# Optimization experiments

Measured on AMD Instinct MI355X. Metric: run time of the kernel, lower is better.

Reference implementation:

```python
import jax, jax.numpy as jnp
import numpy as np
from jax import lax

B, S, D = 4, 4096, 2048
R, E, K, H = 256, 8, 2, 512
MAX_BLEND = 0.9


def setup_inputs() -> dict:
    key = jax.random.key(0)
    ks = jax.random.split(key, 11)
    def w(k, shape, fan_in):
        return jax.random.normal(k, shape, dtype=jnp.float32) * (1.0 / np.sqrt(fan_in))
    return {
        "h": jax.random.normal(ks[0], (B, S, D), dtype=jnp.float32),
        "V": w(ks[1], (D, R), D),            # down-projection (z = V^T h)
        "U": w(ks[2], (R, D), R),            # reconstruction (h = U z)
        "Wr": w(ks[3], (R, E), R),           # router
        "br": jnp.zeros((E,), dtype=jnp.float32),
        "W1": w(ks[4], (E, R, H), R),        # per-expert up-proj
        "b1": jnp.zeros((E, H), dtype=jnp.float32),
        "W2": w(ks[5], (E, H, R), H),        # per-expert down-proj
        "b2": jnp.zeros((E, R), dtype=jnp.float32),
        "Wh": w(ks[6], (D, 1), D),           # halting unit
        "bh": jnp.zeros((1,), dtype=jnp.float32),
    }


def _forward(h, V, U, Wr, br, W1, b1, W2, b2, Wh, bh):
    b, s, d = h.shape
    T = b * s
    # 1. project to vein subspace: z = V^T h  -> [B,S,R]
    z = jnp.einsum("bsd,dr->bsr", h, V)
    zf = z.reshape(T, R)
    # 2. top-k routing
    logits = zf @ Wr + br                      # [T,E]
    probs = jax.nn.softmax(logits, axis=-1)
    topw, topi = lax.top_k(probs, K)           # [T,K]
    topw = topw / jnp.sum(topw, axis=-1, keepdims=True)
    combine = jnp.zeros((T, E), dtype=zf.dtype).at[jnp.arange(T)[:, None], topi].add(topw)
    # 3. expert mix (dense-compute reference; combine is K-sparse per token)
    hidden = jax.nn.gelu(jnp.einsum("tr,erh->teh", zf, W1) + b1, approximate=False)
    expert_out = jnp.einsum("teh,ehr->ter", hidden, W2) + b2    # [T,E,R]
    z_new = jnp.einsum("te,ter->tr", combine, expert_out).reshape(b, s, R)
    # 4. residual blend: blend = min(top_k/num_experts, max_blend)
    blend = min(K / E, MAX_BLEND)
    z_final = z_new * blend + z * (1.0 - blend)
    # 5. reconstruct + halting
    h_new = jnp.einsum("bsr,rd->bsd", z_final, U)
    p_halt = jax.nn.sigmoid(jnp.einsum("bsd,do->bso", h_new, Wh) + bh)
    return h_new, p_halt


def reference(h, V, U, Wr, br, W1, b1, W2, b2, Wh, bh):
    return _forward(h, V, U, Wr, br, W1, b1, W2, b2, Wh, bh)
```

## Files before the change

kernel.cpp:

```cpp
#include <hip/hip_runtime.h>
#include <stdint.h>
#include <math.h>

#define TK 16384
#define DD 2048
#define RR 256
#define EE 8
#define HH 512
#define NSEG_MAX 264
#define NPAIR_MAX (NSEG_MAX * 128)

typedef __attribute__((ext_vector_type(4))) float f32x4;
typedef __attribute__((ext_vector_type(8))) short s16x8;
typedef __attribute__((ext_vector_type(8))) unsigned short u16x8;
typedef __attribute__((ext_vector_type(4))) unsigned u32x4;
typedef unsigned short ushort_t;

__device__ inline unsigned short f2bf(float f) {
  union { float f; unsigned u; } v; v.f = f;
  unsigned r = v.u + 0x7fffu + ((v.u >> 16) & 1u);
  return (unsigned short)(r >> 16);
}
__device__ inline float bf2f(ushort_t u) {
  union { unsigned u; float f; } v; v.u = ((unsigned)u) << 16; return v.f;
}

__device__ inline void gll16(const void* g, void* l) {
  __builtin_amdgcn_global_load_lds(
      (const __attribute__((address_space(1))) void*)g,
      (__attribute__((address_space(3))) void*)l, 16, 0, 0);
}

__device__ inline u16x8 pack8(f32x4 a, f32x4 b) {
  u16x8 r;
  r[0] = f2bf(a.x); r[1] = f2bf(a.y); r[2] = f2bf(a.z); r[3] = f2bf(a.w);
  r[4] = f2bf(b.x); r[5] = f2bf(b.y); r[6] = f2bf(b.z); r[7] = f2bf(b.w);
  return r;
}

#define SWZ8(idx) (((idx & 7) ^ ((idx >> 3) & 7)) * 8)

__global__ __launch_bounds__(256) void k_prep(
    const float* __restrict__ V, const float* __restrict__ U,
    const float* __restrict__ W1, const float* __restrict__ W2,
    const float* __restrict__ Wr, const float* __restrict__ Wh,
    ushort_t* __restrict__ Vt, ushort_t* __restrict__ Ut,
    ushort_t* __restrict__ W1t, ushort_t* __restrict__ W2t,
    float* __restrict__ VeffT, float* __restrict__ Uh) {
  __shared__ float sm[2112];
  int b = blockIdx.x, t = threadIdx.x;
  if (b < 3072) {
    const float* src; ushort_t* dst; int nr, nc, c0, r0;
    if (b < 512)       { src = V; dst = Vt; nr = 2048; nc = 256;
                         c0 = (b & 7) * 32; r0 = (b >> 3) * 32; }
    else if (b < 1024) { int bx = b - 512; src = U; dst = Ut; nr = 256; nc = 2048;
                         c0 = (bx & 63) * 32; r0 = (bx >> 6) * 32; }
    else if (b < 2048) { int bx = b - 1024; int s = bx >> 7; bx &= 127;
                         src = W1 + (size_t)s * 131072; dst = W1t + (size_t)s * 131072;
                         nr = 256; nc = 512; c0 = (bx & 15) * 32; r0 = (bx >> 4) * 32; }
    else               { int bx = b - 2048; int s = bx >> 7; bx &= 127;
                         src = W2 + (size_t)s * 131072; dst = W2t + (size_t)s * 131072;
                         nr = 512; nc = 256; c0 = (bx & 7) * 32; r0 = (bx >> 3) * 32; }
    int tx = t & 31, ty = t >> 5;
    #pragma unroll
    for (int i = 0; i < 32; i += 8)
      sm[(ty + i) * 33 + tx] = src[(size_t)(r0 + ty + i) * nc + c0 + tx];
    __syncthreads();
    #pragma unroll
    for (int i = 0; i < 32; i += 8)
      dst[(size_t)(c0 + ty + i) * nr + r0 + tx] = f2bf(sm[tx * 33 + ty + i]);
  } else if (b < 3080) {
    #pragma unroll
    for (int i = 0; i < 8; ++i) sm[i * 256 + t] = Wr[i * 256 + t];
    __syncthreads();
    int d = (b - 3072) * 256 + t;
    float a[8] = {0, 0, 0, 0, 0, 0, 0, 0};
    const float* vrow = V + (size_t)d * RR;
    for (int r = 0; r < RR; r += 4) {
      f32x4 v = *(const f32x4*)(vrow + r);
      #pragma unroll
      for (int e = 0; e < 8; ++e)
        a[e] += v.x * sm[r * 8 + e] + v.y * sm[(r + 1) * 8 + e] +
                v.z * sm[(r + 2) * 8 + e] + v.w * sm[(r + 3) * 8 + e];
    }
    #pragma unroll
    for (int e = 0; e < 8; ++e) VeffT[(size_t)e * DD + d] = a[e];
  } else {
    int wave = t >> 6, lane = t & 63;
    int r = (b - 3080) * 4 + wave;
    const f32x4* u4 = (const f32x4*)(U + (size_t)r * DD);
    const f32x4* w4 = (const f32x4*)Wh;
    float acc = 0.f;
    #pragma unroll
    for (int it = 0; it < 8; ++it) {
      f32x4 a = u4[it * 64 + lane], bb = w4[it * 64 + lane];
      acc += a.x * bb.x + a.y * bb.y + a.z * bb.z + a.w * bb.w;
    }
    #pragma unroll
    for (int o = 32; o; o >>= 1) acc += __shfl_down(acc, o, 64);
    if (lane == 0) Uh[r] = acc;
  }
}

__global__ __launch_bounds__(256, 2) void k_front(
    const float* __restrict__ h, const ushort_t* __restrict__ Vt,
    const float* __restrict__ VeffT, const float* __restrict__ br,
    ushort_t* __restrict__ zb, int* __restrict__ topi, float* __restrict__ topw,
    int* __restrict__ ctrl) {
  __shared__ ushort_t As[2][32 * 72];
  __shared__ ushort_t Bs[2][256 * 64];
  __shared__ float Vs[2][512];
  __shared__ int lcnt[8];
  int t = threadIdx.x;
  int m0 = blockIdx.x * 32;
  int lane = t & 63, wave = t >> 6;
  int ln = lane & 15, hi = lane >> 4;
  const int xo = (ln & 7) << 3;
  int arow = t >> 3, koff = (t & 7) * 8;
  const float* aptr = h + (size_t)(m0 + arow) * DD + koff;
  if (t < 8) lcnt[t] = 0;

  f32x4 acc[2][4];
  #pragma unroll
  for (int i = 0; i < 2; ++i)
    #pragma unroll
    for (int j = 0; j < 4; ++j) acc[i][j] = (f32x4){0.f, 0.f, 0.f, 0.f};
  float racc[8] = {0, 0, 0, 0, 0, 0, 0, 0};

  f32x4 pc0, pc1, pn0, pn1;
  {
    pc0 = ((const f32x4*)aptr)[0];
    pc1 = ((const f32x4*)aptr)[1];
    #pragma unroll
    for (int u = 0; u < 8; ++u) {
      int idx = u * 256 + t;
      gll16(Vt + (size_t)(idx >> 3) * DD + SWZ8(idx), &Bs[0][idx * 8]);
    }
    if (t < 128) gll16(VeffT + (size_t)(t >> 4) * DD + (t & 15) * 4, &Vs[0][t * 4]);
    *(u16x8*)&As[0][arow * 72 + koff] = pack8(pc0, pc1);
  }
  __syncthreads();

  for (int s = 0; s < 32; ++s) {
    int cb = s & 1, xb = cb ^ 1;
    int k1 = (s + 1) * 64;
    if (s < 31) {
      pn0 = ((const f32x4*)(aptr + k1))[0];
      pn1 = ((const f32x4*)(aptr + k1))[1];
      #pragma unroll
      for (int u = 0; u < 8; ++u) {
        int idx = u * 256 + t;
        gll16(Vt + (size_t)(idx >> 3) * DD + k1 + SWZ8(idx), &Bs[xb][idx * 8]);
      }
      if (t < 128) gll16(VeffT + (size_t)(t >> 4) * DD + k1 + (t & 15) * 4, &Vs[xb][t * 4]);
    }
    {
      const f32x4* vsb = (const f32x4*)&Vs[cb][0];
      #pragma unroll
      for (int e = 0; e < 8; ++e) {
        f32x4 v0 = vsb[(e * 64 + koff) >> 2];
        f32x4 v1 = vsb[((e * 64 + koff) >> 2) + 1];
        racc[e] += pc0.x * v0.x + pc0.y * v0.y + pc0.z * v0.z + pc0.w * v0.w +
                   pc1.x * v1.x + pc1.y * v1.y + pc1.z * v1.z + pc1.w * v1.w;
      }
    }
    #pragma unroll
    for (int ks = 0; ks < 2; ++ks) {
      s16x8 af[2], bq[4];
      #pragma unroll
      for (int i = 0; i < 2; ++i)
        af[i] = *(const s16x8*)&As[cb][(i * 16 + ln) * 72 + ks * 32 + hi * 8];
      #pragma unroll
      for (int j = 0; j < 4; ++j)
        bq[j] = *(const s16x8*)&Bs[cb][(wave * 64 + j * 16 + ln) * 64 + ((ks * 32 + hi * 8) ^ xo)];
      #pragma unroll
      for (int i = 0; i < 2; ++i)
        #pragma unroll
        for (int j = 0; j < 4; ++j)
          acc[i][j] = __builtin_amdgcn_mfma_f32_16x16x32_bf16(af[i], bq[j], acc[i][j], 0, 0, 0);
    }
    if (s < 31) {
      *(u16x8*)&As[xb][arow * 72 + koff] = pack8(pn0, pn1);
      pc0 = pn0; pc1 = pn1;
    }
    __syncthreads();
  }

  #pragma unroll
  for (int i = 0; i < 2; ++i)
    #pragma unroll
    for (int j = 0; j < 4; ++j)
      #pragma unroll
      for (int r = 0; r < 4; ++r) {
        int row = m0 + i * 16 + hi * 4 + r;
        int col = wave * 64 + j * 16 + ln;
        zb[(size_t)row * RR + col] = f2bf(acc[i][j][r]);
      }

  #pragma unroll
  for (int e = 0; e < 8; ++e) {
    racc[e] += __shfl_xor(racc[e], 1, 64);
    racc[e] += __shfl_xor(racc[e], 2, 64);
    racc[e] += __shfl_xor(racc[e], 4, 64);
  }
  if ((t & 7) == 0) {
    int token = m0 + arow;
    f32x4 br0 = ((const f32x4*)br)[0], br1 = ((const f32x4*)br)[1];
    float l[8] = {racc[0] + br0.x, racc[1] + br0.y, racc[2] + br0.z, racc[3] + br0.w,
                  racc[4] + br1.x, racc[5] + br1.y, racc[6] + br1.z, racc[7] + br1.w};
    float best = -1e30f; int bi = 0;
    #pragma unroll
    for (int e = 0; e < 8; ++e) if (l[e] > best) { best = l[e]; bi = e; }
    float sec = -1e30f; int si = 0;
    #pragma unroll
    for (int e = 0; e < 8; ++e) if (e != bi && l[e] > sec) { sec = l[e]; si = e; }
    float w0 = 1.f / (1.f + expf(sec - best));
    topi[token * 2 + 0] = bi; topi[token * 2 + 1] = si;
    topw[token * 2 + 0] = w0; topw[token * 2 + 1] = 1.f - w0;
    atomicAdd(&lcnt[bi], 1);
    atomicAdd(&lcnt[si], 1);
  }
  __syncthreads();
  if (t < 8) atomicAdd(&ctrl[t], lcnt[t]);
}

__global__ __launch_bounds__(256) void k_bases(int* ctrl) {
  __shared__ int sb[8], se[8];
  int t = threadIdx.x;
  if (t < 8) {
    int segs = (ctrl[t] + 127) >> 7;
    int scan = segs;
    #pragma unroll
    for (int o = 1; o < 8; o <<= 1) {
      int u2 = __shfl_up(scan, o, 64);
      if (t >= o) scan += u2;
    }
    int start = scan - segs;
    ctrl[8 + t] = start << 7;
    sb[t] = start; se[t] = scan;
  }
  __syncthreads();
  for (int sg = t; sg < NSEG_MAX; sg += 256) {
    int e = -1;
    #pragma unroll
    for (int k = 0; k < 8; ++k)
      if (sg >= sb[k] && sg < se[k]) e = k;
    ctrl[16 + sg] = e;
  }
}

__global__ __launch_bounds__(256) void k_scatter(const int* topi, const float* topw,
                                                 int* ctrl, int* pair_t, float* pair_w,
                                                 int* inv) {
  __shared__ int lcnt[8], lbase[8];
  int t = threadIdx.x;
  if (t < 8) lcnt[t] = 0;
  __syncthreads();
  int slot = blockIdx.x * 256 + t;
  int e = topi[slot];
  float wv = topw[slot];
  int lp = atomicAdd(&lcnt[e], 1);
  __syncthreads();
  if (t < 8) lbase[t] = atomicAdd(&ctrl[8 + t], lcnt[t]);
  __syncthreads();
  int p = lbase[e] + lp;
  pair_t[p] = slot >> 1;
  pair_w[p] = wv;
  inv[slot] = p;
}

#define GEMM_COMPUTE(AS, BS)                                                          \
  _Pragma("unroll")                                                                   \
  for (int ks = 0; ks < 2; ++ks) {                                                    \
    s16x8 af[4], bq[4];                                                               \
    _Pragma("unroll")                                                                 \
    for (int i = 0; i < 4; ++i)                                                       \
      af[i] = *(const s16x8*)&AS[(wr * 64 + i * 16 + ln) * 64 + ((ks * 32 + hi * 8) ^ xo)]; \
    _Pragma("unroll")                                                                 \
    for (int j = 0; j < 4; ++j)                                                       \
      bq[j] = *(const s16x8*)&BS[(wc * 64 + j * 16 + ln) * 64 + ((ks * 32 + hi * 8) ^ xo)]; \
    _Pragma("unroll")                                                                 \
    for (int i = 0; i < 4; ++i)                                                       \
      _Pragma("unroll")                                                               \
      for (int j = 0; j < 4; ++j)                                                     \
        acc[i][j] = __builtin_amdgcn_mfma_f32_16x16x32_bf16(af[i], bq[j], acc[i][j], 0, 0, 0); \
  }

__global__ __launch_bounds__(256, 2) void k_e1(const ushort_t* zb, const ushort_t* W1t,
                                               const float* b1, const int* ctrl,
                                               const int* pair_t, ushort_t* hidden) {
  __shared__ ushort_t As[2][8192];
  __shared__ ushort_t Bs[2][8192];
  __shared__ int pt[128];
  int sg = blockIdx.x >> 2, nt = blockIdx.x & 3;
  int e = ctrl[16 + sg];
  if (e < 0) return;
  int t = threadIdx.x;
  if (t < 128) pt[t] = pair_t[sg * 128 + t];
  __syncthreads();
  int n0 = nt * 128;
  const ushort_t* Bbase = W1t + (size_t)e * HH * RR;
  int lane = t & 63, wave = t >> 6;
  int wr = wave >> 1, wc = wave & 1;
  int ln = lane & 15, hi = lane >> 4;
  const int xo = (ln & 7) << 3;

  f32x4 acc[4][4];
  #pragma unroll
  for (int i = 0; i < 4; ++i)
    #pragma unroll
    for (int j = 0; j < 4; ++j) acc[i][j] = (f32x4){0.f, 0.f, 0.f, 0.f};

  #pragma unroll
  for (int u = 0; u < 4; ++u) {
    int idx = u * 256 + t;
    gll16(zb + (size_t)pt[idx >> 3] * RR + SWZ8(idx), &As[0][idx * 8]);
    gll16(Bbase + (size_t)(n0 + (idx >> 3)) * RR + SWZ8(idx), &Bs[0][idx * 8]);
  }
  __syncthreads();
  for (int s = 0; s < 4; ++s) {
    int cb = s & 1, xb = cb ^ 1;
    if (s < 3) {
      int k1 = (s + 1) * 64;
      #pragma unroll
      for (int u = 0; u < 4; ++u) {
        int idx = u * 256 + t;
        gll16(zb + (size_t)pt[idx >> 3] * RR + k1 + SWZ8(idx), &As[xb][idx * 8]);
        gll16(Bbase + (size_t)(n0 + (idx >> 3)) * RR + k1 + SWZ8(idx), &Bs[xb][idx * 8]);
      }
    }
    GEMM_COMPUTE(As[cb], Bs[cb]);
    __syncthreads();
  }
  #pragma unroll
  for (int i = 0; i < 4; ++i)
    #pragma unroll
    for (int j = 0; j < 4; ++j)
      #pragma unroll
      for (int r = 0; r < 4; ++r) {
        int pl = wr * 64 + i * 16 + hi * 4 + r;
        int col = n0 + wc * 64 + j * 16 + ln;
        float v = acc[i][j][r] + b1[e * HH + col];
        float g = 0.5f * v * (1.f + erff(v * 0.70710678118654752f));
        hidden[(size_t)(sg * 128 + pl) * HH + col] = f2bf(g);
      }
}

__global__ __launch_bounds__(256, 2) void k_e2(const ushort_t* hidden, const ushort_t* W2t,
                                               const float* b2, const int* ctrl,
                                               const int* pair_t, const float* pair_w,
                                               ushort_t* eout) {
  __shared__ ushort_t As[2][8192];
  __shared__ ushort_t Bs[2][8192];
  __shared__ float pw[128];
  int sg = blockIdx.x >> 1, nt = blockIdx.x & 1;
  int e = ctrl[16 + sg];
  if (e < 0) return;
  int t = threadIdx.x;
  if (t < 128) pw[t] = pair_w[sg * 128 + t];
  __syncthreads();
  int n0 = nt * 128;
  const ushort_t* Abase = hidden + (size_t)sg * 128 * HH;
  const ushort_t* Bbase = W2t + (size_t)e * RR * HH;
  int lane = t & 63, wave = t >> 6;
  int wr = wave >> 1, wc = wave & 1;
  int ln = lane & 15, hi = lane >> 4;
  const int xo = (ln & 7) << 3;

  f32x4 acc[4][4];
  #pragma unroll
  for (int i = 0; i < 4; ++i)
    #pragma unroll
    for (int j = 0; j < 4; ++j) acc[i][j] = (f32x4){0.f, 0.f, 0.f, 0.f};

  #pragma unroll
  for (int u = 0; u < 4; ++u) {
    int idx = u * 256 + t;
    gll16(Abase + (size_t)(idx >> 3) * HH + SWZ8(idx), &As[0][idx * 8]);
    gll16(Bbase + (size_t)(n0 + (idx >> 3)) * HH + SWZ8(idx), &Bs[0][idx * 8]);
  }
  __syncthreads();
  for (int s = 0; s < 8; ++s) {
    int cb = s & 1, xb = cb ^ 1;
    if (s < 7) {
      int k1 = (s + 1) * 64;
      #pragma unroll
      for (int u = 0; u < 4; ++u) {
        int idx = u * 256 + t;
        gll16(Abase + (size_t)(idx >> 3) * HH + k1 + SWZ8(idx), &As[xb][idx * 8]);
        gll16(Bbase + (size_t)(n0 + (idx >> 3)) * HH + k1 + SWZ8(idx), &Bs[xb][idx * 8]);
      }
    }
    GEMM_COMPUTE(As[cb], Bs[cb]);
    __syncthreads();
  }
  #pragma unroll
  for (int i = 0; i < 4; ++i)
    #pragma unroll
    for (int j = 0; j < 4; ++j)
      #pragma unroll
      for (int r = 0; r < 4; ++r) {
        int pl = wr * 64 + i * 16 + hi * 4 + r;
        int col = n0 + wc * 64 + j * 16 + ln;
        float v = acc[i][j][r] + b2[e * RR + col];
        eout[(size_t)(sg * 128 + pl) * RR + col] = f2bf(pw[pl] * v);
      }
}

__global__ __launch_bounds__(256) void k_final(const ushort_t* __restrict__ zb,
                                               const ushort_t* __restrict__ eout,
                                               const int* __restrict__ inv,
                                               const float* __restrict__ Uh,
                                               const float* __restrict__ bh,
                                               ushort_t* __restrict__ zb2,
                                               float* __restrict__ phalt) {
  __shared__ float luh[256];
  int t = threadIdx.x;
  if (t < 64) ((f32x4*)luh)[t] = ((const f32x4*)Uh)[t];
  __syncthreads();
  int tok = blockIdx.x * 64 + (t >> 2), q = t & 3;
  int i0 = inv[tok * 2], i1 = inv[tok * 2 + 1];
  const u16x8* z8 = (const u16x8*)(zb + (size_t)tok * RR + q * 64);
  const u16x8* ea = (const u16x8*)(eout + (size_t)i0 * RR + q * 64);
  const u16x8* eb = (const u16x8*)(eout + (size_t)i1 * RR + q * 64);
  ushort_t* o = zb2 + (size_t)tok * RR + q * 64;
  float acc = 0.f;
  #pragma unroll
  for (int it = 0; it < 8; ++it) {
    u16x8 zv = z8[it], av = ea[it], bv = eb[it];
    u16x8 pk;
    #pragma unroll
    for (int j = 0; j < 8; ++j) {
      float zf = 0.75f * bf2f(zv[j]) + 0.25f * (bf2f(av[j]) + bf2f(bv[j]));
      acc += zf * luh[q * 64 + it * 8 + j];
      pk[j] = f2bf(zf);
    }
    *(u16x8*)(o + it * 8) = pk;
  }
  acc += __shfl_xor(acc, 1, 64);
  acc += __shfl_xor(acc, 2, 64);
  if (q == 0) phalt[tok] = 1.f / (1.f + expf(-(acc + bh[0])));
}

__global__ __launch_bounds__(256, 2) void k_gemm_u(const ushort_t* zb2, const ushort_t* Ut,
                                                   float* outp) {
  __shared__ ushort_t As[2][8192];
  __shared__ ushort_t Bs[2][8192];
  int hw = blockIdx.x;
  int bid = (hw & 7) * 256 + (hw >> 3);
  int mt = bid >> 4, nt = bid & 15;
  int m0 = mt * 128, n0 = nt * 128;
  int t = threadIdx.x;
  int lane = t & 63, wave = t >> 6;
  int wr = wave >> 1, wc = wave & 1;
  int ln = lane & 15, hi = lane >> 4;
  const int xo = (ln & 7) << 3;

  f32x4 acc[4][4];
  #pragma unroll
  for (int i = 0; i < 4; ++i)
    #pragma unroll
    for (int j = 0; j < 4; ++j) acc[i][j] = (f32x4){0.f, 0.f, 0.f, 0.f};

  #pragma unroll
  for (int u = 0; u < 4; ++u) {
    int idx = u * 256 + t;
    gll16(zb2 + (size_t)(m0 + (idx >> 3)) * RR + SWZ8(idx), &As[0][idx * 8]);
    gll16(Ut + (size_t)(n0 + (idx >> 3)) * RR + SWZ8(idx), &Bs[0][idx * 8]);
  }
  __syncthreads();
  for (int s = 0; s < 4; ++s) {
    int cb = s & 1, xb = cb ^ 1;
    if (s < 3) {
      int k1 = (s + 1) * 64;
      #pragma unroll
      for (int u = 0; u < 4; ++u) {
        int idx = u * 256 + t;
        gll16(zb2 + (size_t)(m0 + (idx >> 3)) * RR + k1 + SWZ8(idx), &As[xb][idx * 8]);
        gll16(Ut + (size_t)(n0 + (idx >> 3)) * RR + k1 + SWZ8(idx), &Bs[xb][idx * 8]);
      }
    }
    GEMM_COMPUTE(As[cb], Bs[cb]);
    __syncthreads();
  }
  #pragma unroll
  for (int i = 0; i < 4; ++i)
    #pragma unroll
    for (int j = 0; j < 4; ++j)
      #pragma unroll
      for (int r = 0; r < 4; ++r) {
        int row = m0 + wr * 64 + i * 16 + hi * 4 + r;
        int col = n0 + wc * 64 + j * 16 + ln;
        outp[(size_t)row * DD + col] = acc[i][j][r];
      }
}

extern "C" void kernel_launch(void* const* d_in, const int* in_sizes, int n_in,
                              void* d_out, int out_size, void* d_ws, size_t ws_size,
                              hipStream_t stream) {
  (void)in_sizes; (void)n_in; (void)out_size;
  const float* h  = (const float*)d_in[0];
  const float* V  = (const float*)d_in[1];
  const float* U  = (const float*)d_in[2];
  const float* Wr = (const float*)d_in[3];
  const float* br = (const float*)d_in[4];
  const float* W1 = (const float*)d_in[5];
  const float* b1 = (const float*)d_in[6];
  const float* W2 = (const float*)d_in[7];
  const float* b2 = (const float*)d_in[8];
  const float* Wh = (const float*)d_in[9];
  const float* bh = (const float*)d_in[10];
  float* outp = (float*)d_out;
  char* w = (char*)d_ws;

  constexpr size_t OFF_VT    = 0;
  constexpr size_t OFF_UT    = 1048576;
  constexpr size_t OFF_W1T   = 2097152;
  constexpr size_t OFF_W2T   = 4194304;
  constexpr size_t OFF_VEFFT = 6291456;
  constexpr size_t OFF_UHV   = 6356992;
  constexpr size_t OFF_TOPI  = 6361088;
  constexpr size_t OFF_TOPW  = 6492160;
  constexpr size_t OFF_INV   = 6623232;
  constexpr size_t OFF_CTRL  = 6754304;
  constexpr size_t OFF_PT    = 6758400;
  constexpr size_t OFF_PW    = 6893568;
  constexpr size_t OFF_ZB    = 7028736;
  constexpr size_t OFF_EOUT  = 15417344;
  constexpr size_t OFF_HID   = 32718848;
  constexpr size_t OFF_ZB2   = OFF_HID;
  constexpr size_t WS_NEED   = 67321856;
  if (ws_size < WS_NEED) return;

  ushort_t* Vt    = (ushort_t*)(w + OFF_VT);
  ushort_t* Ut    = (ushort_t*)(w + OFF_UT);
  ushort_t* W1t   = (ushort_t*)(w + OFF_W1T);
  ushort_t* W2t   = (ushort_t*)(w + OFF_W2T);
  float*    VeffT = (float*)(w + OFF_VEFFT);
  float*    Uh    = (float*)(w + OFF_UHV);
  int*      topi  = (int*)(w + OFF_TOPI);
  float*    topw  = (float*)(w + OFF_TOPW);
  int*      inv   = (int*)(w + OFF_INV);
  int*      ctrl  = (int*)(w + OFF_CTRL);
  int*      pair_t= (int*)(w + OFF_PT);
  float*    pair_w= (float*)(w + OFF_PW);
  ushort_t* zb    = (ushort_t*)(w + OFF_ZB);
  ushort_t* eout  = (ushort_t*)(w + OFF_EOUT);
  ushort_t* hidden= (ushort_t*)(w + OFF_HID);
  ushort_t* zb2   = (ushort_t*)(w + OFF_ZB2);

  hipMemsetAsync(w + OFF_CTRL, 0, OFF_ZB - OFF_CTRL, stream);

  k_prep<<<3144, 256, 0, stream>>>(V, U, W1, W2, Wr, Wh, Vt, Ut, W1t, W2t, VeffT, Uh);
  k_front<<<512, 256, 0, stream>>>(h, Vt, VeffT, br, zb, topi, topw, ctrl);
  k_bases<<<1, 256, 0, stream>>>(ctrl);
  k_scatter<<<128, 256, 0, stream>>>(topi, topw, ctrl, pair_t, pair_w, inv);
  k_e1<<<NSEG_MAX * 4, 256, 0, stream>>>(zb, W1t, b1, ctrl, pair_t, hidden);
  k_e2<<<NSEG_MAX * 2, 256, 0, stream>>>(hidden, W2t, b2, ctrl, pair_t, pair_w, eout);
  k_final<<<256, 256, 0, stream>>>(zb, eout, inv, Uh, bh, zb2, outp + (size_t)TK * DD);
  k_gemm_u<<<2048, 256, 0, stream>>>(zb2, Ut, outp);
}
```

Measured before the change: 220.6 us.

## Split front projection across two N-halves and fold memset into prep kernel

The front GEMM (h·V) now launches 1024 blocks, each computing a 32x128 output tile instead of 32x256. Block indices are swizzled so the two N-halves of the same M-tile run on different groups. Only the nt==0 half computes the router logits and top-k, and the smaller LDS footprint allows raising occupancy to 3 blocks per SIMD. The hipMemsetAsync that cleared the control and counter region is replaced by extra zeroing blocks in k_prep, saving one launch. As a trade-off, the fp32 h activations are now read twice, and the router work is unbalanced between the two halves.

```diff
diff --git a/kernel.cpp b/kernel.cpp
--- a/kernel.cpp
+++ b/kernel.cpp
@@ -46,7 +46,8 @@
     const float* __restrict__ Wr, const float* __restrict__ Wh,
     ushort_t* __restrict__ Vt, ushort_t* __restrict__ Ut,
     ushort_t* __restrict__ W1t, ushort_t* __restrict__ W2t,
-    float* __restrict__ VeffT, float* __restrict__ Uh) {
+    float* __restrict__ VeffT, float* __restrict__ Uh,
+    u32x4* __restrict__ zbase) {
   __shared__ float sm[2112];
   int b = blockIdx.x, t = threadIdx.x;
   if (b < 3072) {
@@ -85,7 +86,7 @@
     }
     #pragma unroll
     for (int e = 0; e < 8; ++e) VeffT[(size_t)e * DD + d] = a[e];
-  } else {
+  } else if (b < 3144) {
     int wave = t >> 6, lane = t & 63;
     int r = (b - 3080) * 4 + wave;
     const f32x4* u4 = (const f32x4*)(U + (size_t)r * DD);
@@ -99,20 +100,26 @@
     #pragma unroll
     for (int o = 32; o; o >>= 1) acc += __shfl_down(acc, o, 64);
     if (lane == 0) Uh[r] = acc;
-  }
-}
-
-__global__ __launch_bounds__(256, 2) void k_front(
+  } else {
+    int i = (b - 3144) * 256 + t;
+    zbase[i] = (u32x4){0u, 0u, 0u, 0u};
+  }
+}
+
+__global__ __launch_bounds__(256, 3) void k_front(
     const float* __restrict__ h, const ushort_t* __restrict__ Vt,
     const float* __restrict__ VeffT, const float* __restrict__ br,
     ushort_t* __restrict__ zb, int* __restrict__ topi, float* __restrict__ topw,
     int* __restrict__ ctrl) {
   __shared__ ushort_t As[2][32 * 72];
-  __shared__ ushort_t Bs[2][256 * 64];
+  __shared__ ushort_t Bs[2][128 * 64];
   __shared__ float Vs[2][512];
   __shared__ int lcnt[8];
-  int t = threadIdx.x;
-  int m0 = blockIdx.x * 32;
+  int hw = blockIdx.x;
+  int swz = (hw & 7) * 128 + (hw >> 3);
+  int mt = swz >> 1, nt = swz & 1;
+  int m0 = mt * 32, n0 = nt * 128;
+  int t = threadIdx.x;
   int lane = t & 63, wave = t >> 6;
   int ln = lane & 15, hi = lane >> 4;
   const int xo = (ln & 7) << 3;
@@ -120,11 +127,11 @@
   const float* aptr = h + (size_t)(m0 + arow) * DD + koff;
   if (t < 8) lcnt[t] = 0;
 
-  f32x4 acc[2][4];
+  f32x4 acc[2][2];
   #pragma unroll
   for (int i = 0; i < 2; ++i)
     #pragma unroll
-    for (int j = 0; j < 4; ++j) acc[i][j] = (f32x4){0.f, 0.f, 0.f, 0.f};
+    for (int j = 0; j < 2; ++j) acc[i][j] = (f32x4){0.f, 0.f, 0.f, 0.f};
   float racc[8] = {0, 0, 0, 0, 0, 0, 0, 0};
 
   f32x4 pc0, pc1, pn0, pn1;
@@ -132,11 +139,11 @@
     pc0 = ((const f32x4*)aptr)[0];
     pc1 = ((const f32x4*)aptr)[1];
     #pragma unroll
-    for (int u = 0; u < 8; ++u) {
+    for (int u = 0; u < 4; ++u) {
       int idx = u * 256 + t;
-      gll16(Vt + (size_t)(idx >> 3) * DD + SWZ8(idx), &Bs[0][idx * 8]);
-    }
-    if (t < 128) gll16(VeffT + (size_t)(t >> 4) * DD + (t & 15) * 4, &Vs[0][t * 4]);
+      gll16(Vt + (size_t)(n0 + (idx >> 3)) * DD + SWZ8(idx), &Bs[0][idx * 8]);
+    }
+    if (nt == 0 && t < 128) gll16(VeffT + (size_t)(t >> 4) * DD + (t & 15) * 4, &Vs[0][t * 4]);
     *(u16x8*)&As[0][arow * 72 + koff] = pack8(pc0, pc1);
   }
   __syncthreads();
@@ -148,13 +155,14 @@
       pn0 = ((const f32x4*)(aptr + k1))[0];
       pn1 = ((const f32x4*)(aptr + k1))[1];
       #pragma unroll
-      for (int u = 0; u < 8; ++u) {
+      for (int u = 0; u < 4; ++u) {
         int idx = u * 256 + t;
-        gll16(Vt + (size_t)(idx >> 3) * DD + k1 + SWZ8(idx), &Bs[xb][idx * 8]);
-      }
-      if (t < 128) gll16(VeffT + (size_t)(t >> 4) * DD + k1 + (t & 15) * 4, &Vs[xb][t * 4]);
-    }
-    {
+        gll16(Vt + (size_t)(n0 + (idx >> 3)) * DD + k1 + SWZ8(idx), &Bs[xb][idx * 8]);
+      }
+      if (nt == 0 && t < 128)
+        gll16(VeffT + (size_t)(t >> 4) * DD + k1 + (t & 15) * 4, &Vs[xb][t * 4]);
+    }
+    if (nt == 0) {
       const f32x4* vsb = (const f32x4*)&Vs[cb][0];
       #pragma unroll
       for (int e = 0; e < 8; ++e) {
@@ -166,17 +174,17 @@
     }
     #pragma unroll
     for (int ks = 0; ks < 2; ++ks) {
-      s16x8 af[2], bq[4];
+      s16x8 af[2], bq[2];
       #pragma unroll
       for (int i = 0; i < 2; ++i)
         af[i] = *(const s16x8*)&As[cb][(i * 16 + ln) * 72 + ks * 32 + hi * 8];
       #pragma unroll
-      for (int j = 0; j < 4; ++j)
-        bq[j] = *(const s16x8*)&Bs[cb][(wave * 64 + j * 16 + ln) * 64 + ((ks * 32 + hi * 8) ^ xo)];
+      for (int j = 0; j < 2; ++j)
+        bq[j] = *(const s16x8*)&Bs[cb][(wave * 32 + j * 16 + ln) * 64 + ((ks * 32 + hi * 8) ^ xo)];
       #pragma unroll
       for (int i = 0; i < 2; ++i)
         #pragma unroll
-        for (int j = 0; j < 4; ++j)
+        for (int j = 0; j < 2; ++j)
           acc[i][j] = __builtin_amdgcn_mfma_f32_16x16x32_bf16(af[i], bq[j], acc[i][j], 0, 0, 0);
     }
     if (s < 31) {
@@ -189,39 +197,41 @@
   #pragma unroll
   for (int i = 0; i < 2; ++i)
     #pragma unroll
-    for (int j = 0; j < 4; ++j)
+    for (int j = 0; j < 2; ++j)
       #pragma unroll
       for (int r = 0; r < 4; ++r) {
         int row = m0 + i * 16 + hi * 4 + r;
-        int col = wave * 64 + j * 16 + ln;
+        int col = n0 + wave * 32 + j * 16 + ln;
         zb[(size_t)row * RR + col] = f2bf(acc[i][j][r]);
       }
 
-  #pragma unroll
-  for (int e = 0; e < 8; ++e) {
-    racc[e] += __shfl_xor(racc[e], 1, 64);
-    racc[e] += __shfl_xor(racc[e], 2, 64);
-    racc[e] += __shfl_xor(racc[e], 4, 64);
-  }
-  if ((t & 7) == 0) {
-    int token = m0 + arow;
-    f32x4 br0 = ((const f32x4*)br)[0], br1 = ((const f32x4*)br)[1];
-    float l[8] = {racc[0] + br0.x, racc[1] + br0.y, racc[2] + br0.z, racc[3] + br0.w,
-                  racc[4] + br1.x, racc[5] + br1.y, racc[6] + br1.z, racc[7] + br1.w};
-    float best = -1e30f; int bi = 0;
-    #pragma unroll
-    for (int e = 0; e < 8; ++e) if (l[e] > best) { best = l[e]; bi = e; }
-    float sec = -1e30f; int si = 0;
-    #pragma unroll
-    for (int e = 0; e < 8; ++e) if (e != bi && l[e] > sec) { sec = l[e]; si = e; }
-    float w0 = 1.f / (1.f + expf(sec - best));
-    topi[token * 2 + 0] = bi; topi[token * 2 + 1] = si;
-    topw[token * 2 + 0] = w0; topw[token * 2 + 1] = 1.f - w0;
-    atomicAdd(&lcnt[bi], 1);
-    atomicAdd(&lcnt[si], 1);
-  }
-  __syncthreads();
-  if (t < 8) atomicAdd(&ctrl[t], lcnt[t]);
+  if (nt == 0) {
+    #pragma unroll
+    for (int e = 0; e < 8; ++e) {
+      racc[e] += __shfl_xor(racc[e], 1, 64);
+      racc[e] += __shfl_xor(racc[e], 2, 64);
+      racc[e] += __shfl_xor(racc[e], 4, 64);
+    }
+    if ((t & 7) == 0) {
+      int token = m0 + arow;
+      f32x4 br0 = ((const f32x4*)br)[0], br1 = ((const f32x4*)br)[1];
+      float l[8] = {racc[0] + br0.x, racc[1] + br0.y, racc[2] + br0.z, racc[3] + br0.w,
+                    racc[4] + br1.x, racc[5] + br1.y, racc[6] + br1.z, racc[7] + br1.w};
+      float best = -1e30f; int bi = 0;
+      #pragma unroll
+      for (int e = 0; e < 8; ++e) if (l[e] > best) { best = l[e]; bi = e; }
+      float sec = -1e30f; int si = 0;
+      #pragma unroll
+      for (int e = 0; e < 8; ++e) if (e != bi && l[e] > sec) { sec = l[e]; si = e; }
+      float w0 = 1.f / (1.f + expf(sec - best));
+      topi[token * 2 + 0] = bi; topi[token * 2 + 1] = si;
+      topw[token * 2 + 0] = w0; topw[token * 2 + 1] = 1.f - w0;
+      atomicAdd(&lcnt[bi], 1);
+      atomicAdd(&lcnt[si], 1);
+    }
+    __syncthreads();
+    if (t < 8) atomicAdd(&ctrl[t], lcnt[t]);
+  }
 }
 
 __global__ __launch_bounds__(256) void k_bases(int* ctrl) {
@@ -549,10 +559,9 @@
   ushort_t* hidden= (ushort_t*)(w + OFF_HID);
   ushort_t* zb2   = (ushort_t*)(w + OFF_ZB2);
 
-  hipMemsetAsync(w + OFF_CTRL, 0, OFF_ZB - OFF_CTRL, stream);
-
-  k_prep<<<3144, 256, 0, stream>>>(V, U, W1, W2, Wr, Wh, Vt, Ut, W1t, W2t, VeffT, Uh);
-  k_front<<<512, 256, 0, stream>>>(h, Vt, VeffT, br, zb, topi, topw, ctrl);
+  k_prep<<<3211, 256, 0, stream>>>(V, U, W1, W2, Wr, Wh, Vt, Ut, W1t, W2t,
+                                   VeffT, Uh, (u32x4*)(w + OFF_CTRL));
+  k_front<<<1024, 256, 0, stream>>>(h, Vt, VeffT, br, zb, topi, topw, ctrl);
   k_bases<<<1, 256, 0, stream>>>(ctrl);
   k_scatter<<<128, 256, 0, stream>>>(topi, topw, ctrl, pair_t, pair_w, inv);
   k_e1<<<NSEG_MAX * 4, 256, 0, stream>>>(zb, W1t, b1, ctrl, pair_t, hidden);
```

Result: slower. 241.0 us (+9.3%).
